# Optimization experiments

Hardware: AMD Instinct MI355X
Metric: run time of the kernel (lower is better)

Reference implementation:

```python
import jax, jax.numpy as jnp
import numpy as np

N, S, D, H = 2, 2048, 1024, 16
DH = D // H  # 64


def setup_inputs() -> dict:
    key = jax.random.key(0)
    ks = jax.random.split(key, 7)
    scale = 1.0 / np.sqrt(DH)  # ~nn.Linear default init range
    return {
        "sequences": jax.random.normal(ks[0], (N, S, D), dtype=jnp.float32),
        "Wq": jax.random.uniform(ks[1], (H, DH, DH), jnp.float32, -scale, scale),
        "bq": jax.random.uniform(ks[2], (H, DH), jnp.float32, -scale, scale),
        "Wk": jax.random.uniform(ks[3], (H, DH, DH), jnp.float32, -scale, scale),
        "bk": jax.random.uniform(ks[4], (H, DH), jnp.float32, -scale, scale),
        "Wv": jax.random.uniform(ks[5], (H, DH, DH), jnp.float32, -scale, scale),
        "bv": jax.random.uniform(ks[6], (H, DH), jnp.float32, -scale, scale),
    }


def reference(sequences, Wq, bq, Wk, bk, Wv, bv):
    n, s, d = sequences.shape
    x = sequences.reshape(n, s, H, DH)  # [N,S,H,Dh]
    # per-head Linear: y = x @ W^T + b, batched over heads
    q = jnp.einsum('nshd,hed->nshe', x, Wq) + bq  # [N,S,H,Dh]
    k = jnp.einsum('nshd,hed->nshe', x, Wk) + bk
    v = jnp.einsum('nshd,hed->nshe', x, Wv) + bv
    # attention: scores [N,H,S,S]
    scores = jnp.einsum('nqhd,nkhd->nhqk', q, k) / jnp.sqrt(jnp.float32(DH))
    w = jax.nn.softmax(scores, axis=-1)
    out = jnp.einsum('nhqk,nkhd->nqhd', w, v)  # [N,S,H,Dh]
    return out.reshape(n, s, d)
```

## Files before the change

### kernel.cpp

```cpp
#include <hip/hip_runtime.h>
#include <hip/hip_bf16.h>


#define NB 2
#define SS 2048
#define DM 1024
#define NH 16
#define DHd 64

typedef __attribute__((ext_vector_type(8))) short bf16x8;
typedef __attribute__((ext_vector_type(4))) float f32x4;

union U8 { bf16x8 v; unsigned short u[8]; };

__device__ __forceinline__ unsigned short f2b(float x) {
    __hip_bfloat16 h = __float2bfloat16(x);
    return *reinterpret_cast<unsigned short*>(&h);
}

__device__ __forceinline__ bf16x8 pack8(float4 a, float4 b) {
    U8 t;
    t.u[0] = f2b(a.x); t.u[1] = f2b(a.y); t.u[2] = f2b(a.z); t.u[3] = f2b(a.w);
    t.u[4] = f2b(b.x); t.u[5] = f2b(b.y); t.u[6] = f2b(b.z); t.u[7] = f2b(b.w);
    return t.v;
}

__device__ __forceinline__ int swz(int row, int ch) {
    return row * 64 + ((ch ^ (row & 7)) * 8);
}

#define QSCALE 0.18033688011112042f

__global__ __launch_bounds__(256) void qkv_proj(
    const float* __restrict__ seq,
    const float* __restrict__ Wq, const float* __restrict__ bq,
    const float* __restrict__ Wk, const float* __restrict__ bk,
    const float* __restrict__ Wv, const float* __restrict__ bv,
    unsigned short* __restrict__ Q, unsigned short* __restrict__ K,
    unsigned short* __restrict__ Vt)
{
    __shared__ unsigned short Xl[128 * 64];
    __shared__ unsigned short Wl[3 * 64 * 64];
    __shared__ unsigned short Ol[128 * 72];

    const int tid = threadIdx.x;
    const int wv = tid >> 6, L = tid & 63, lo = L & 15, qd = L >> 4;
    const int bi = blockIdx.x;
    const int nh = bi >> 4, sb = bi & 15;
    const int h = nh & (NH - 1), n = nh >> 4;
    const int s0 = sb * 128;

#pragma unroll
    for (int i = 0; i < 4; ++i) {
        int idx = tid + i * 256;
        int r = idx >> 3, ch = idx & 7;
        const float* src = seq + ((size_t)(n * SS + s0 + r)) * DM + h * DHd + ch * 8;
        float4 a = ((const float4*)src)[0];
        float4 b = ((const float4*)src)[1];
        *(bf16x8*)&Xl[swz(r, ch)] = pack8(a, b);
    }
#pragma unroll
    for (int i = 0; i < 6; ++i) {
        int idx = tid + i * 256;
        int mat = idx >> 9;
        int rem = idx & 511;
        int e = rem >> 3, ch = rem & 7;
        const float* Wm = (mat == 0) ? Wq : (mat == 1) ? Wk : Wv;
        const float* src = Wm + (size_t)(h * DHd + e) * DHd + ch * 8;
        float4 a = ((const float4*)src)[0];
        float4 b = ((const float4*)src)[1];
        *(bf16x8*)&Wl[mat * 4096 + swz(e, ch)] = pack8(a, b);
    }
    __syncthreads();

    bf16x8 xf[2][2];
#pragma unroll
    for (int st = 0; st < 2; ++st)
#pragma unroll
        for (int kt = 0; kt < 2; ++kt)
            xf[st][kt] = *(const bf16x8*)&Xl[swz(wv * 32 + st * 16 + lo, kt * 4 + qd)];

#pragma unroll
    for (int m2 = 0; m2 < 2; ++m2) {
        const unsigned short* Wb = &Wl[m2 * 4096];
        const float* bias = m2 ? bk : bq;
        unsigned short* O = m2 ? K : Q;
        const float sc = m2 ? 1.0f : QSCALE;

        f32x4 acc[4][2];
#pragma unroll
        for (int et = 0; et < 4; ++et) {
            float4 bb = *(const float4*)&bias[h * DHd + et * 16 + qd * 4];
#pragma unroll
            for (int st = 0; st < 2; ++st)
                acc[et][st] = (f32x4){bb.x, bb.y, bb.z, bb.w};
        }
#pragma unroll
        for (int et = 0; et < 4; ++et) {
            bf16x8 wf0 = *(const bf16x8*)&Wb[swz(et * 16 + lo, qd)];
            bf16x8 wf1 = *(const bf16x8*)&Wb[swz(et * 16 + lo, 4 + qd)];
#pragma unroll
            for (int st = 0; st < 2; ++st) {
                acc[et][st] = __builtin_amdgcn_mfma_f32_16x16x32_bf16(
                    wf0, xf[st][0], acc[et][st], 0, 0, 0);
                acc[et][st] = __builtin_amdgcn_mfma_f32_16x16x32_bf16(
                    wf1, xf[st][1], acc[et][st], 0, 0, 0);
            }
        }
        if (m2) __syncthreads();
#pragma unroll
        for (int et = 0; et < 4; ++et)
#pragma unroll
            for (int st = 0; st < 2; ++st) {
                int s = wv * 32 + st * 16 + lo;
                ushort4 w;
                w.x = f2b(acc[et][st][0] * sc); w.y = f2b(acc[et][st][1] * sc);
                w.z = f2b(acc[et][st][2] * sc); w.w = f2b(acc[et][st][3] * sc);
                *(ushort4*)&Ol[s * 72 + et * 16 + qd * 4] = w;
            }
        __syncthreads();
        {
            const int sl = tid >> 3, e0 = (tid & 7) * 8;
#pragma unroll
            for (int i = 0; i < 4; ++i) {
                bf16x8 v = *(const bf16x8*)&Ol[(i * 32 + sl) * 72 + e0];
                *(bf16x8*)&O[((size_t)nh * SS + s0 + i * 32 + sl) * DHd + e0] = v;
            }
        }
    }

    {
        const unsigned short* Wb = &Wl[2 * 4096];
        float bvv[4];
#pragma unroll
        for (int et = 0; et < 4; ++et) bvv[et] = bv[h * DHd + et * 16 + lo];

        f32x4 acc[2][4];
#pragma unroll
        for (int st = 0; st < 2; ++st)
#pragma unroll
            for (int et = 0; et < 4; ++et)
                acc[st][et] = (f32x4){bvv[et], bvv[et], bvv[et], bvv[et]};
#pragma unroll
        for (int et = 0; et < 4; ++et) {
            bf16x8 wf0 = *(const bf16x8*)&Wb[swz(et * 16 + lo, qd)];
            bf16x8 wf1 = *(const bf16x8*)&Wb[swz(et * 16 + lo, 4 + qd)];
#pragma unroll
            for (int st = 0; st < 2; ++st) {
                acc[st][et] = __builtin_amdgcn_mfma_f32_16x16x32_bf16(
                    xf[st][0], wf0, acc[st][et], 0, 0, 0);
                acc[st][et] = __builtin_amdgcn_mfma_f32_16x16x32_bf16(
                    xf[st][1], wf1, acc[st][et], 0, 0, 0);
            }
        }
        __syncthreads();
#pragma unroll
        for (int st = 0; st < 2; ++st)
#pragma unroll
            for (int et = 0; et < 4; ++et) {
                int e = et * 16 + lo;
                int s = wv * 32 + st * 16 + qd * 4;
                ushort4 w;
                w.x = f2b(acc[st][et][0]); w.y = f2b(acc[st][et][1]);
                w.z = f2b(acc[st][et][2]); w.w = f2b(acc[st][et][3]);
                *(ushort4*)&Ol[e * 136 + s] = w;
            }
        __syncthreads();
        {
            const int er = tid >> 4, s8 = (tid & 15) * 8;
#pragma unroll
            for (int i = 0; i < 4; ++i) {
                int e = i * 16 + er;
                bf16x8 v = *(const bf16x8*)&Ol[e * 136 + s8];
                *(bf16x8*)&Vt[((size_t)nh * DHd + e) * SS + s0 + s8] = v;
            }
        }
    }
}

#define PSTR 72
#define NT (SS / 64)

__global__ __launch_bounds__(256) void attn(
    const unsigned short* __restrict__ Qg, const unsigned short* __restrict__ Kg,
    const unsigned short* __restrict__ Vg, float* __restrict__ out)
{
    __shared__ unsigned short Kl[2][64 * 64];
    __shared__ unsigned short Vl[2][64 * 64];
    __shared__ unsigned short Pl[4][32 * PSTR];

    const int tid = threadIdx.x;
    const int wv = tid >> 6, L = tid & 63, lo = L & 15, qd = L >> 4;

    const int orig = blockIdx.x;
    const int xcd = orig & 7, slot = orig >> 3;
    const int nh = xcd * 4 + (slot >> 4);
    const int qblk = slot & 15;
    const int h = nh & (NH - 1), n = nh >> 4;
    const int q0 = qblk * 128 + wv * 32;

    const unsigned short* Qnh = Qg + (size_t)nh * SS * DHd;
    const unsigned short* Knh = Kg + (size_t)nh * SS * DHd;
    const unsigned short* Vnh = Vg + (size_t)nh * DHd * SS;

    const int r0 = tid >> 3, c0 = tid & 7;

    bf16x8 qf[2][2];
#pragma unroll
    for (int ct = 0; ct < 2; ++ct)
#pragma unroll
        for (int kt = 0; kt < 2; ++kt)
            qf[ct][kt] = *(const bf16x8*)(Qnh + (size_t)(q0 + ct * 16 + lo) * DHd
                                          + kt * 32 + qd * 8);

    f32x4 oacc[4][2];
#pragma unroll
    for (int rt = 0; rt < 4; ++rt)
#pragma unroll
        for (int ct = 0; ct < 2; ++ct)
            oacc[rt][ct] = (f32x4){0.f, 0.f, 0.f, 0.f};

    float l[2] = {0.f, 0.f};

    uint4 ks0 = *(const uint4*)(Knh + (size_t)r0 * DHd + c0 * 8);
    uint4 ks1 = *(const uint4*)(Knh + (size_t)(r0 + 32) * DHd + c0 * 8);
    uint4 vs0 = *(const uint4*)(Vnh + (size_t)r0 * SS + c0 * 8);
    uint4 vs1 = *(const uint4*)(Vnh + (size_t)(r0 + 32) * SS + c0 * 8);
    *(uint4*)&Kl[0][swz(r0, c0)]      = ks0;
    *(uint4*)&Kl[0][swz(r0 + 32, c0)] = ks1;
    *(uint4*)&Vl[0][swz(r0, c0)]      = vs0;
    *(uint4*)&Vl[0][swz(r0 + 32, c0)] = vs1;
    ks0 = *(const uint4*)(Knh + (size_t)(64 + r0) * DHd + c0 * 8);
    ks1 = *(const uint4*)(Knh + (size_t)(64 + r0 + 32) * DHd + c0 * 8);
    vs0 = *(const uint4*)(Vnh + (size_t)r0 * SS + 64 + c0 * 8);
    vs1 = *(const uint4*)(Vnh + (size_t)(r0 + 32) * SS + 64 + c0 * 8);
    __syncthreads();

    for (int t = 0; t < NT; ++t) {
        const int cur = t & 1;

        f32x4 sacc[4][2];
#pragma unroll
        for (int rt = 0; rt < 4; ++rt)
#pragma unroll
            for (int ct = 0; ct < 2; ++ct)
                sacc[rt][ct] = (f32x4){0.f, 0.f, 0.f, 0.f};
        __builtin_amdgcn_s_setprio(1);
#pragma unroll
        for (int rt = 0; rt < 4; ++rt)
#pragma unroll
            for (int kt = 0; kt < 2; ++kt) {
                bf16x8 kf = *(const bf16x8*)&Kl[cur][swz(rt * 16 + lo, kt * 4 + qd)];
#pragma unroll
                for (int ct = 0; ct < 2; ++ct)
                    sacc[rt][ct] = __builtin_amdgcn_mfma_f32_16x16x32_bf16(
                        kf, qf[ct][kt], sacc[rt][ct], 0, 0, 0);
            }
        __builtin_amdgcn_s_setprio(0);

#pragma unroll
        for (int ct = 0; ct < 2; ++ct) {
            float rs = 0.f;
#pragma unroll
            for (int rt = 0; rt < 4; ++rt) {
                float p0 = __builtin_amdgcn_exp2f(sacc[rt][ct][0]);
                float p1 = __builtin_amdgcn_exp2f(sacc[rt][ct][1]);
                float p2 = __builtin_amdgcn_exp2f(sacc[rt][ct][2]);
                float p3 = __builtin_amdgcn_exp2f(sacc[rt][ct][3]);
                rs += (p0 + p1) + (p2 + p3);
                ushort4 w;
                w.x = f2b(p0); w.y = f2b(p1); w.z = f2b(p2); w.w = f2b(p3);
                *(ushort4*)&Pl[wv][(ct * 16 + lo) * PSTR + rt * 16 + qd * 4] = w;
            }
            l[ct] += rs;
        }

        __builtin_amdgcn_s_setprio(1);
#pragma unroll
        for (int kt = 0; kt < 2; ++kt) {
            bf16x8 pfr[2];
#pragma unroll
            for (int ct = 0; ct < 2; ++ct)
                pfr[ct] = *(const bf16x8*)&Pl[wv][(ct * 16 + lo) * PSTR
                                                  + kt * 32 + qd * 8];
#pragma unroll
            for (int rt = 0; rt < 4; ++rt) {
                bf16x8 vf = *(const bf16x8*)&Vl[cur][swz(rt * 16 + lo, kt * 4 + qd)];
#pragma unroll
                for (int ct = 0; ct < 2; ++ct)
                    oacc[rt][ct] = __builtin_amdgcn_mfma_f32_16x16x32_bf16(
                        vf, pfr[ct], oacc[rt][ct], 0, 0, 0);
            }
        }
        __builtin_amdgcn_s_setprio(0);

        if (t + 1 < NT) {
            *(uint4*)&Kl[cur ^ 1][swz(r0, c0)]      = ks0;
            *(uint4*)&Kl[cur ^ 1][swz(r0 + 32, c0)] = ks1;
            *(uint4*)&Vl[cur ^ 1][swz(r0, c0)]      = vs0;
            *(uint4*)&Vl[cur ^ 1][swz(r0 + 32, c0)] = vs1;
            if (t + 2 < NT) {
                const int kn = (t + 2) * 64;
                ks0 = *(const uint4*)(Knh + (size_t)(kn + r0) * DHd + c0 * 8);
                ks1 = *(const uint4*)(Knh + (size_t)(kn + r0 + 32) * DHd + c0 * 8);
                vs0 = *(const uint4*)(Vnh + (size_t)r0 * SS + kn + c0 * 8);
                vs1 = *(const uint4*)(Vnh + (size_t)(r0 + 32) * SS + kn + c0 * 8);
            }
        }
        __syncthreads();
    }

#pragma unroll
    for (int ct = 0; ct < 2; ++ct) {
        float lt = l[ct];
        lt += __shfl_xor(lt, 16, 64);
        lt += __shfl_xor(lt, 32, 64);
        const float inv = 1.0f / lt;
        const int s = q0 + ct * 16 + lo;
#pragma unroll
        for (int rt = 0; rt < 4; ++rt) {
            float4 o;
            o.x = oacc[rt][ct][0] * inv; o.y = oacc[rt][ct][1] * inv;
            o.z = oacc[rt][ct][2] * inv; o.w = oacc[rt][ct][3] * inv;
            *(float4*)&out[((size_t)n * SS + s) * DM + h * DHd
                           + rt * 16 + qd * 4] = o;
        }
    }
}

extern "C" void kernel_launch(void* const* d_in, const int* in_sizes, int n_in,
                              void* d_out, int out_size, void* d_ws, size_t ws_size,
                              hipStream_t stream) {
    const float* seq = (const float*)d_in[0];
    const float* Wq  = (const float*)d_in[1];
    const float* bq  = (const float*)d_in[2];
    const float* Wk  = (const float*)d_in[3];
    const float* bk  = (const float*)d_in[4];
    const float* Wv  = (const float*)d_in[5];
    const float* bv  = (const float*)d_in[6];
    float* out = (float*)d_out;

    const size_t per = (size_t)NB * NH * SS * DHd;
    unsigned short* Q  = (unsigned short*)d_ws;
    unsigned short* K  = Q + per;
    unsigned short* Vt = K + per;

    qkv_proj<<<512, 256, 0, stream>>>(seq, Wq, bq, Wk, bk, Wv, bv, Q, K, Vt);
    attn<<<512, 256, 0, stream>>>(Q, K, Vt, out);
}
```

Before: 135.7 us.

## Compute softmax row sums via MFMA and interleave exp with PV matmul

The per-lane scalar row-sum adds and the cross-lane shuffles are replaced with an extra MFMA against a ones vector that accumulates the row sums of the bf16 probabilities. V fragments are preloaded into registers before the next-tile LDS stores, so the exp and P write for each column tile can overlap with the PV MFMAs of the other column tile. The aim is to cut VALU work and give the scheduler more overlap. The cost is more registers for the V fragments and two extra MFMAs per column tile. The denominator is now summed from bf16-rounded probabilities rather than fp32 values.

```diff
diff --git a/kernel.cpp b/kernel.cpp
--- a/kernel.cpp
+++ b/kernel.cpp
@@ -220,7 +220,17 @@
         for (int ct = 0; ct < 2; ++ct)
             oacc[rt][ct] = (f32x4){0.f, 0.f, 0.f, 0.f};
 
-    float l[2] = {0.f, 0.f};
+    f32x4 racc[2];
+    racc[0] = (f32x4){0.f, 0.f, 0.f, 0.f};
+    racc[1] = (f32x4){0.f, 0.f, 0.f, 0.f};
+    bf16x8 ones;
+    {
+        U8 t;
+        unsigned short o = (lo == 0) ? (unsigned short)0x3F80 : (unsigned short)0;
+#pragma unroll
+        for (int j = 0; j < 8; ++j) t.u[j] = o;
+        ones = t.v;
+    }
 
     uint4 ks0 = *(const uint4*)(Knh + (size_t)r0 * DHd + c0 * 8);
     uint4 ks1 = *(const uint4*)(Knh + (size_t)(r0 + 32) * DHd + c0 * 8);
@@ -258,41 +268,12 @@
             }
         __builtin_amdgcn_s_setprio(0);
 
-#pragma unroll
-        for (int ct = 0; ct < 2; ++ct) {
-            float rs = 0.f;
-#pragma unroll
-            for (int rt = 0; rt < 4; ++rt) {
-                float p0 = __builtin_amdgcn_exp2f(sacc[rt][ct][0]);
-                float p1 = __builtin_amdgcn_exp2f(sacc[rt][ct][1]);
-                float p2 = __builtin_amdgcn_exp2f(sacc[rt][ct][2]);
-                float p3 = __builtin_amdgcn_exp2f(sacc[rt][ct][3]);
-                rs += (p0 + p1) + (p2 + p3);
-                ushort4 w;
-                w.x = f2b(p0); w.y = f2b(p1); w.z = f2b(p2); w.w = f2b(p3);
-                *(ushort4*)&Pl[wv][(ct * 16 + lo) * PSTR + rt * 16 + qd * 4] = w;
-            }
-            l[ct] += rs;
-        }
-
-        __builtin_amdgcn_s_setprio(1);
-#pragma unroll
-        for (int kt = 0; kt < 2; ++kt) {
-            bf16x8 pfr[2];
-#pragma unroll
-            for (int ct = 0; ct < 2; ++ct)
-                pfr[ct] = *(const bf16x8*)&Pl[wv][(ct * 16 + lo) * PSTR
-                                                  + kt * 32 + qd * 8];
-#pragma unroll
-            for (int rt = 0; rt < 4; ++rt) {
-                bf16x8 vf = *(const bf16x8*)&Vl[cur][swz(rt * 16 + lo, kt * 4 + qd)];
-#pragma unroll
-                for (int ct = 0; ct < 2; ++ct)
-                    oacc[rt][ct] = __builtin_amdgcn_mfma_f32_16x16x32_bf16(
-                        vf, pfr[ct], oacc[rt][ct], 0, 0, 0);
-            }
-        }
-        __builtin_amdgcn_s_setprio(0);
+        bf16x8 vfr[2][4];
+#pragma unroll
+        for (int kt = 0; kt < 2; ++kt)
+#pragma unroll
+            for (int rt = 0; rt < 4; ++rt)
+                vfr[kt][rt] = *(const bf16x8*)&Vl[cur][swz(rt * 16 + lo, kt * 4 + qd)];
 
         if (t + 1 < NT) {
             *(uint4*)&Kl[cur ^ 1][swz(r0, c0)]      = ks0;
@@ -307,14 +288,43 @@
                 vs1 = *(const uint4*)(Vnh + (size_t)(r0 + 32) * SS + kn + c0 * 8);
             }
         }
+
+#pragma unroll
+        for (int ct = 0; ct < 2; ++ct) {
+#pragma unroll
+            for (int rt = 0; rt < 4; ++rt) {
+                float p0 = __builtin_amdgcn_exp2f(sacc[rt][ct][0]);
+                float p1 = __builtin_amdgcn_exp2f(sacc[rt][ct][1]);
+                float p2 = __builtin_amdgcn_exp2f(sacc[rt][ct][2]);
+                float p3 = __builtin_amdgcn_exp2f(sacc[rt][ct][3]);
+                ushort4 w;
+                w.x = f2b(p0); w.y = f2b(p1); w.z = f2b(p2); w.w = f2b(p3);
+                *(ushort4*)&Pl[wv][(ct * 16 + lo) * PSTR + rt * 16 + qd * 4] = w;
+            }
+            bf16x8 pfr[2];
+#pragma unroll
+            for (int kt = 0; kt < 2; ++kt)
+                pfr[kt] = *(const bf16x8*)&Pl[wv][(ct * 16 + lo) * PSTR
+                                                  + kt * 32 + qd * 8];
+            __builtin_amdgcn_s_setprio(1);
+#pragma unroll
+            for (int kt = 0; kt < 2; ++kt) {
+#pragma unroll
+                for (int rt = 0; rt < 4; ++rt)
+                    oacc[rt][ct] = __builtin_amdgcn_mfma_f32_16x16x32_bf16(
+                        vfr[kt][rt], pfr[kt], oacc[rt][ct], 0, 0, 0);
+                racc[ct] = __builtin_amdgcn_mfma_f32_16x16x32_bf16(
+                    ones, pfr[kt], racc[ct], 0, 0, 0);
+            }
+            __builtin_amdgcn_s_setprio(0);
+        }
+
         __syncthreads();
     }
 
 #pragma unroll
     for (int ct = 0; ct < 2; ++ct) {
-        float lt = l[ct];
-        lt += __shfl_xor(lt, 16, 64);
-        lt += __shfl_xor(lt, 32, 64);
+        const float lt = __shfl(racc[ct][0], lo, 64);
         const float inv = 1.0f / lt;
         const int s = q0 + ct * 16 + lo;
 #pragma unroll
```

Result: no change. 137.3 us (+1.2%).
